# Performance work log

Measured on AMD Instinct MI355X. Metric: run time of the kernel, lower is better.

Reference implementation:

```python
import jax, jax.numpy as jnp
import numpy as np

T = 100.0  # temperature, from init_kwargs
B = 4096
D = 128
NUM_CLASSES = 10


def setup_inputs() -> dict:
    key = jax.random.key(0)
    kx, ky = jax.random.split(key)
    x = jax.random.normal(kx, (B, D), dtype=jnp.float32)
    y = jax.random.randint(ky, (B,), 0, NUM_CLASSES, dtype=jnp.int64)
    return {"x": x, "y": y}


def reference(x, y):
    # Pairwise squared Euclidean distances: dist[i,j] = ||x_i - x_j||^2
    sq = jnp.sum(x * x, axis=1)                      # [b]
    dist = sq[:, None] + sq[None, :] - 2.0 * (x @ x.T)  # [b, b]
    dist = jnp.maximum(dist, 0.0)                    # clamp fp error; diag -> 0

    e = jnp.exp(-dist / T)                           # [b, b]; e[i,i] = 1

    b = x.shape[0]
    same = (y[:, None] == y[None, :])                # same-label mask
    not_self = ~jnp.eye(b, dtype=bool)

    # numerator: sum over j != i with y[j] == y[i]
    num = jnp.sum(jnp.where(same & not_self, e, 0.0), axis=1)  # [b]
    # denominator: sum over ALL j, including j == i (exp(0) = 1), as in the
    # original loop where the denominator accumulates unconditionally
    den = jnp.sum(e, axis=1)                         # [b]

    return jnp.mean(-jnp.log(num / den))
```

## Files before the change

### kernel.cpp

```cpp
#include <hip/hip_runtime.h>
#include <hip/hip_bf16.h>

#define NB 4096

typedef short v8s __attribute__((ext_vector_type(8)));
typedef float v4f __attribute__((ext_vector_type(4)));


__global__ __launch_bounds__(256) void prep_kernel(const float* __restrict__ x,
        float* __restrict__ sq, unsigned short* __restrict__ xb,
        float* __restrict__ out) {
    int tid = threadIdx.x;
    int row = blockIdx.x * 8 + (tid >> 5);
    int lane = tid & 31;
    const float4* xg = (const float4*)x;
    float4 v = xg[row * 32 + lane];
    __hip_bfloat16 h0 = __float2bfloat16(v.x), h1 = __float2bfloat16(v.y);
    __hip_bfloat16 h2 = __float2bfloat16(v.z), h3 = __float2bfloat16(v.w);
    ushort4 u4;
    u4.x = *(unsigned short*)&h0; u4.y = *(unsigned short*)&h1;
    u4.z = *(unsigned short*)&h2; u4.w = *(unsigned short*)&h3;
    ((ushort4*)xb)[row * 32 + lane] = u4;
    float f0 = __bfloat162float(h0), f1 = __bfloat162float(h1);
    float f2 = __bfloat162float(h2), f3 = __bfloat162float(h3);
    float s = f0 * f0 + f1 * f1 + f2 * f2 + f3 * f3;
    #pragma unroll
    for (int off = 16; off > 0; off >>= 1) s += __shfl_down(s, off);
    if (lane == 0) sq[row] = s;
    if (blockIdx.x == 0 && tid == 0) out[0] = 0.f;
}

__global__ __launch_bounds__(512, 4) void snn_mfma(const unsigned short* __restrict__ xb,
        const int* __restrict__ y, const float* __restrict__ sqg,
        float2* __restrict__ part) {
    __shared__ __align__(16) unsigned short At[128 * 136];
    __shared__ __align__(16) unsigned short Bt[128 * 136];
    __shared__ float2 red[2][128];
    __shared__ float sqi[128], sqj[128];
    __shared__ int yi[128], yj[128];

    const int tid = threadIdx.x;
    const int w    = tid >> 6;
    const int lane = tid & 63;
    const int wm = w >> 1;
    const int wn = w & 1;
    const int lr = lane & 15;
    const int q  = lane >> 4;
    const int i0 = blockIdx.x * 128;
    const int j0 = blockIdx.y * 128;

    const v8s* xg = (const v8s*)xb;
    #pragma unroll
    for (int it = 0; it < 4; ++it) {
        int c = it * 512 + tid;
        int row = c >> 4, cc = c & 15;
        *(v8s*)&At[row * 136 + cc * 8] = xg[(i0 + row) * 16 + cc];
        *(v8s*)&Bt[row * 136 + cc * 8] = xg[(j0 + row) * 16 + cc];
    }
    if (tid < 128)      { sqi[tid] = sqg[i0 + tid];       yi[tid] = y[i0 + tid]; }
    else if (tid < 256) { sqj[tid - 128] = sqg[j0 + tid - 128];
                          yj[tid - 128] = y[j0 + tid - 128]; }
    __syncthreads();

    v4f acc[2][4];
    #pragma unroll
    for (int mt = 0; mt < 2; ++mt)
        #pragma unroll
        for (int nt = 0; nt < 4; ++nt)
            #pragma unroll
            for (int r = 0; r < 4; ++r) acc[mt][nt][r] = 0.f;

    #pragma unroll
    for (int kk = 0; kk < 4; ++kk) {
        v8s af[2], bf[4];
        #pragma unroll
        for (int mt = 0; mt < 2; ++mt)
            af[mt] = *(const v8s*)&At[(wm * 32 + mt * 16 + lr) * 136 + kk * 32 + q * 8];
        #pragma unroll
        for (int nt = 0; nt < 4; ++nt)
            bf[nt] = *(const v8s*)&Bt[(wn * 64 + nt * 16 + lr) * 136 + kk * 32 + q * 8];
        #pragma unroll
        for (int mt = 0; mt < 2; ++mt)
            #pragma unroll
            for (int nt = 0; nt < 4; ++nt)
                acc[mt][nt] = __builtin_amdgcn_mfma_f32_16x16x32_bf16(
                    af[mt], bf[nt], acc[mt][nt], 0, 0, 0);
    }

    const float c1 = 0.014426950408889634f;
    const float c2 = 0.028853900817778936f;
    float bj[4]; int yj_r[4], jg[4];
    #pragma unroll
    for (int nt = 0; nt < 4; ++nt) {
        int jc = wn * 64 + nt * 16 + lr;
        bj[nt] = -c1 * sqj[jc]; yj_r[nt] = yj[jc]; jg[nt] = j0 + jc;
    }
    #pragma unroll
    for (int mt = 0; mt < 2; ++mt) {
        #pragma unroll
        for (int r = 0; r < 4; ++r) {
            int rloc = wm * 32 + mt * 16 + q * 4 + r;
            float bi = -c1 * sqi[rloc];
            int yir = yi[rloc], ig = i0 + rloc;
            float n = 0.f, d = 0.f;
            #pragma unroll
            for (int nt = 0; nt < 4; ++nt) {
                float arg = fminf(0.f, fmaf(acc[mt][nt][r], c2, bi + bj[nt]));
                float e = __builtin_amdgcn_exp2f(arg);
                d += e;
                bool ok = (yir == yj_r[nt]) && (ig != jg[nt]);
                n += ok ? e : 0.f;
            }
            n += __shfl_xor(n, 1); d += __shfl_xor(d, 1);
            n += __shfl_xor(n, 2); d += __shfl_xor(d, 2);
            n += __shfl_xor(n, 4); d += __shfl_xor(d, 4);
            n += __shfl_xor(n, 8); d += __shfl_xor(d, 8);
            if (lr == 0) red[wn][rloc] = make_float2(n, d);
        }
    }
    __syncthreads();

    if (tid < 128) {
        float2 a = red[0][tid], b = red[1][tid];
        part[(i0 + tid) * 32 + blockIdx.y] = make_float2(a.x + b.x, a.y + b.y);
    }
}

__global__ __launch_bounds__(256) void snn_final(const float2* __restrict__ part,
        float* __restrict__ out) {
    __shared__ float wsum[4];
    int row = blockIdx.x * 256 + threadIdx.x;
    const float4* p = (const float4*)&part[row * 32];
    float n = 0.f, d = 0.f;
    #pragma unroll
    for (int c = 0; c < 16; ++c) {
        float4 v = p[c];
        n += v.x + v.z; d += v.y + v.w;
    }
    float l = __logf(d) - __logf(n);
    #pragma unroll
    for (int off = 32; off > 0; off >>= 1) l += __shfl_down(l, off);
    int wid = threadIdx.x >> 6;
    if ((threadIdx.x & 63) == 0) wsum[wid] = l;
    __syncthreads();
    if (threadIdx.x == 0) {
        float s = wsum[0] + wsum[1] + wsum[2] + wsum[3];
        atomicAdd(out, s * (1.0f / NB));
    }
}

extern "C" void kernel_launch(void* const* d_in, const int* in_sizes, int n_in,
                              void* d_out, int out_size, void* d_ws, size_t ws_size,
                              hipStream_t stream) {
    const float* x = (const float*)d_in[0];
    const int*   y = (const int*)d_in[1];
    float* out = (float*)d_out;
    float2* part = (float2*)d_ws;
    float* sq = (float*)((char*)d_ws + (1 << 20));
    unsigned short* xb = (unsigned short*)((char*)d_ws + (1 << 20) + (16 << 10));

    prep_kernel<<<NB / 8, 256, 0, stream>>>(x, sq, xb, out);
    dim3 grid(NB / 128, NB / 128);
    snn_mfma<<<grid, 512, 0, stream>>>(xb, y, sq, part);
    snn_final<<<NB / 256, 256, 0, stream>>>(part, out);
}
```

Before: 76.17 us.

## Use direct-to-LDS loads, XOR-swizzled layout, and two j-tiles per block

Xb is now stored with an XOR swizzle on 16-byte chunks, so the LDS tiles need no padding and avoid bank conflicts. Tiles are loaded with global_load_lds DMA instead of going through registers. Each 256-thread block computes a 128x256 strip by reusing the A tile across two B tiles, with a 64x64 register tile per wave. This halves the grid and the partial-sum traffic in exchange for more accumulator registers and serialized B reloads between the two subtiles.

```diff
diff --git a/kernel.cpp b/kernel.cpp
--- a/kernel.cpp
+++ b/kernel.cpp
@@ -6,6 +6,12 @@
 typedef short v8s __attribute__((ext_vector_type(8)));
 typedef float v4f __attribute__((ext_vector_type(4)));
 
+
+__device__ __forceinline__ void dma16(const unsigned short* g, unsigned short* l) {
+    __builtin_amdgcn_global_load_lds(
+        (const __attribute__((address_space(1))) unsigned int*)g,
+        (__attribute__((address_space(3))) unsigned int*)l, 16, 0, 0);
+}
 
 __global__ __launch_bounds__(256) void prep_kernel(const float* __restrict__ x,
         float* __restrict__ sq, unsigned short* __restrict__ xb,
@@ -20,7 +26,9 @@
     ushort4 u4;
     u4.x = *(unsigned short*)&h0; u4.y = *(unsigned short*)&h1;
     u4.z = *(unsigned short*)&h2; u4.w = *(unsigned short*)&h3;
-    ((ushort4*)xb)[row * 32 + lane] = u4;
+    int c = lane >> 1, half = lane & 1;
+    int p = c ^ (row & 15);
+    *(ushort4*)&xb[(size_t)row * 128 + p * 8 + half * 4] = u4;
     float f0 = __bfloat162float(h0), f1 = __bfloat162float(h1);
     float f2 = __bfloat162float(h2), f3 = __bfloat162float(h3);
     float s = f0 * f0 + f1 * f1 + f2 * f2 + f3 * f3;
@@ -30,99 +38,130 @@
     if (blockIdx.x == 0 && tid == 0) out[0] = 0.f;
 }
 
-__global__ __launch_bounds__(512, 4) void snn_mfma(const unsigned short* __restrict__ xb,
+__global__ __launch_bounds__(256) void snn_mfma(const unsigned short* __restrict__ xb,
         const int* __restrict__ y, const float* __restrict__ sqg,
         float2* __restrict__ part) {
-    __shared__ __align__(16) unsigned short At[128 * 136];
-    __shared__ __align__(16) unsigned short Bt[128 * 136];
+    __shared__ __align__(16) unsigned short At[128 * 128];
+    __shared__ __align__(16) unsigned short Bt[128 * 128];
     __shared__ float2 red[2][128];
     __shared__ float sqi[128], sqj[128];
     __shared__ int yi[128], yj[128];
 
     const int tid = threadIdx.x;
-    const int w    = tid >> 6;
-    const int lane = tid & 63;
-    const int wm = w >> 1;
-    const int wn = w & 1;
-    const int lr = lane & 15;
-    const int q  = lane >> 4;
+    const int w = tid >> 6, lane = tid & 63;
+    const int wm = w >> 1, wn = w & 1;
+    const int lr = lane & 15, q = lane >> 4;
     const int i0 = blockIdx.x * 128;
-    const int j0 = blockIdx.y * 128;
-
-    const v8s* xg = (const v8s*)xb;
-    #pragma unroll
-    for (int it = 0; it < 4; ++it) {
-        int c = it * 512 + tid;
-        int row = c >> 4, cc = c & 15;
-        *(v8s*)&At[row * 136 + cc * 8] = xg[(i0 + row) * 16 + cc];
-        *(v8s*)&Bt[row * 136 + cc * 8] = xg[(j0 + row) * 16 + cc];
-    }
-    if (tid < 128)      { sqi[tid] = sqg[i0 + tid];       yi[tid] = y[i0 + tid]; }
-    else if (tid < 256) { sqj[tid - 128] = sqg[j0 + tid - 128];
-                          yj[tid - 128] = y[j0 + tid - 128]; }
+    const int jt0 = blockIdx.y * 2;
+
+    #pragma unroll
+    for (int r = 0; r < 8; ++r) {
+        int row = w * 32 + r * 4;
+        dma16(xb + (size_t)(i0 + row) * 128 + lane * 8, &At[row * 128]);
+        dma16(xb + (size_t)(jt0 * 128 + row) * 128 + lane * 8, &Bt[row * 128]);
+    }
+    if (tid < 128) { sqi[tid] = sqg[i0 + tid]; yi[tid] = y[i0 + tid]; }
+    else { int c = tid - 128; sqj[c] = sqg[jt0 * 128 + c]; yj[c] = y[jt0 * 128 + c]; }
     __syncthreads();
-
-    v4f acc[2][4];
-    #pragma unroll
-    for (int mt = 0; mt < 2; ++mt)
-        #pragma unroll
-        for (int nt = 0; nt < 4; ++nt)
-            #pragma unroll
-            for (int r = 0; r < 4; ++r) acc[mt][nt][r] = 0.f;
-
-    #pragma unroll
-    for (int kk = 0; kk < 4; ++kk) {
-        v8s af[2], bf[4];
-        #pragma unroll
-        for (int mt = 0; mt < 2; ++mt)
-            af[mt] = *(const v8s*)&At[(wm * 32 + mt * 16 + lr) * 136 + kk * 32 + q * 8];
-        #pragma unroll
-        for (int nt = 0; nt < 4; ++nt)
-            bf[nt] = *(const v8s*)&Bt[(wn * 64 + nt * 16 + lr) * 136 + kk * 32 + q * 8];
-        #pragma unroll
-        for (int mt = 0; mt < 2; ++mt)
-            #pragma unroll
-            for (int nt = 0; nt < 4; ++nt)
-                acc[mt][nt] = __builtin_amdgcn_mfma_f32_16x16x32_bf16(
-                    af[mt], bf[nt], acc[mt][nt], 0, 0, 0);
-    }
 
     const float c1 = 0.014426950408889634f;
     const float c2 = 0.028853900817778936f;
-    float bj[4]; int yj_r[4], jg[4];
-    #pragma unroll
-    for (int nt = 0; nt < 4; ++nt) {
-        int jc = wn * 64 + nt * 16 + lr;
-        bj[nt] = -c1 * sqj[jc]; yj_r[nt] = yj[jc]; jg[nt] = j0 + jc;
-    }
-    #pragma unroll
-    for (int mt = 0; mt < 2; ++mt) {
-        #pragma unroll
-        for (int r = 0; r < 4; ++r) {
-            int rloc = wm * 32 + mt * 16 + q * 4 + r;
-            float bi = -c1 * sqi[rloc];
-            int yir = yi[rloc], ig = i0 + rloc;
-            float n = 0.f, d = 0.f;
+    float nsum[4][4], dsum[4][4];
+    #pragma unroll
+    for (int mt = 0; mt < 4; ++mt)
+        #pragma unroll
+        for (int r = 0; r < 4; ++r) { nsum[mt][r] = 0.f; dsum[mt][r] = 0.f; }
+
+    #pragma unroll
+    for (int jt = 0; jt < 2; ++jt) {
+        v4f acc[4][4];
+        #pragma unroll
+        for (int mt = 0; mt < 4; ++mt)
+            #pragma unroll
+            for (int nt = 0; nt < 4; ++nt)
+                #pragma unroll
+                for (int r = 0; r < 4; ++r) acc[mt][nt][r] = 0.f;
+
+        #pragma unroll
+        for (int kk = 0; kk < 4; ++kk) {
+            v8s af[4], bf[4];
+            #pragma unroll
+            for (int mt = 0; mt < 4; ++mt) {
+                int row = wm * 64 + mt * 16 + lr;
+                af[mt] = *(const v8s*)&At[row * 128 + (((kk * 4 + q) ^ lr) * 8)];
+            }
             #pragma unroll
             for (int nt = 0; nt < 4; ++nt) {
-                float arg = fminf(0.f, fmaf(acc[mt][nt][r], c2, bi + bj[nt]));
-                float e = __builtin_amdgcn_exp2f(arg);
-                d += e;
-                bool ok = (yir == yj_r[nt]) && (ig != jg[nt]);
-                n += ok ? e : 0.f;
-            }
-            n += __shfl_xor(n, 1); d += __shfl_xor(d, 1);
-            n += __shfl_xor(n, 2); d += __shfl_xor(d, 2);
-            n += __shfl_xor(n, 4); d += __shfl_xor(d, 4);
-            n += __shfl_xor(n, 8); d += __shfl_xor(d, 8);
-            if (lr == 0) red[wn][rloc] = make_float2(n, d);
-        }
-    }
+                int row = wn * 64 + nt * 16 + lr;
+                bf[nt] = *(const v8s*)&Bt[row * 128 + (((kk * 4 + q) ^ lr) * 8)];
+            }
+            #pragma unroll
+            for (int mt = 0; mt < 4; ++mt)
+                #pragma unroll
+                for (int nt = 0; nt < 4; ++nt)
+                    acc[mt][nt] = __builtin_amdgcn_mfma_f32_16x16x32_bf16(
+                        af[mt], bf[nt], acc[mt][nt], 0, 0, 0);
+        }
+
+        int jbase = (jt0 + jt) * 128;
+        float bj[4]; int yj_r[4], jcol[4];
+        #pragma unroll
+        for (int nt = 0; nt < 4; ++nt) {
+            int jc = wn * 64 + nt * 16 + lr;
+            bj[nt] = -c1 * sqj[jc]; yj_r[nt] = yj[jc]; jcol[nt] = jbase + jc;
+        }
+        #pragma unroll
+        for (int mt = 0; mt < 4; ++mt) {
+            #pragma unroll
+            for (int r = 0; r < 4; ++r) {
+                int rloc = wm * 64 + mt * 16 + q * 4 + r;
+                float bi = -c1 * sqi[rloc];
+                int yir = yi[rloc], ig = i0 + rloc;
+                float n = 0.f, d = 0.f;
+                #pragma unroll
+                for (int nt = 0; nt < 4; ++nt) {
+                    float arg = fminf(0.f, fmaf(acc[mt][nt][r], c2, bi + bj[nt]));
+                    float e = __builtin_amdgcn_exp2f(arg);
+                    d += e;
+                    bool ok = (yir == yj_r[nt]) && (ig != jcol[nt]);
+                    n += ok ? e : 0.f;
+                }
+                n += __shfl_xor(n, 1); d += __shfl_xor(d, 1);
+                n += __shfl_xor(n, 2); d += __shfl_xor(d, 2);
+                n += __shfl_xor(n, 4); d += __shfl_xor(d, 4);
+                n += __shfl_xor(n, 8); d += __shfl_xor(d, 8);
+                nsum[mt][r] += n; dsum[mt][r] += d;
+            }
+        }
+
+        if (jt == 0) {
+            __syncthreads();
+            #pragma unroll
+            for (int r = 0; r < 8; ++r) {
+                int row = w * 32 + r * 4;
+                dma16(xb + (size_t)((jt0 + 1) * 128 + row) * 128 + lane * 8,
+                      &Bt[row * 128]);
+            }
+            if (tid >= 128) {
+                int c = tid - 128;
+                sqj[c] = sqg[(jt0 + 1) * 128 + c]; yj[c] = y[(jt0 + 1) * 128 + c];
+            }
+            __syncthreads();
+        }
+    }
+
+    #pragma unroll
+    for (int mt = 0; mt < 4; ++mt)
+        #pragma unroll
+        for (int r = 0; r < 4; ++r)
+            if (lr == 0)
+                red[wn][wm * 64 + mt * 16 + q * 4 + r] =
+                    make_float2(nsum[mt][r], dsum[mt][r]);
     __syncthreads();
 
     if (tid < 128) {
         float2 a = red[0][tid], b = red[1][tid];
-        part[(i0 + tid) * 32 + blockIdx.y] = make_float2(a.x + b.x, a.y + b.y);
+        part[(size_t)(i0 + tid) * 16 + blockIdx.y] = make_float2(a.x + b.x, a.y + b.y);
     }
 }
 
@@ -130,10 +169,10 @@
         float* __restrict__ out) {
     __shared__ float wsum[4];
     int row = blockIdx.x * 256 + threadIdx.x;
-    const float4* p = (const float4*)&part[row * 32];
+    const float4* p = (const float4*)&part[(size_t)row * 16];
     float n = 0.f, d = 0.f;
     #pragma unroll
-    for (int c = 0; c < 16; ++c) {
+    for (int c = 0; c < 8; ++c) {
         float4 v = p[c];
         n += v.x + v.z; d += v.y + v.w;
     }
@@ -156,11 +195,11 @@
     const int*   y = (const int*)d_in[1];
     float* out = (float*)d_out;
     float2* part = (float2*)d_ws;
-    float* sq = (float*)((char*)d_ws + (1 << 20));
-    unsigned short* xb = (unsigned short*)((char*)d_ws + (1 << 20) + (16 << 10));
+    float* sq = (float*)((char*)d_ws + (512 << 10));
+    unsigned short* xb = (unsigned short*)((char*)d_ws + (512 << 10) + (16 << 10));
 
     prep_kernel<<<NB / 8, 256, 0, stream>>>(x, sq, xb, out);
-    dim3 grid(NB / 128, NB / 128);
-    snn_mfma<<<grid, 512, 0, stream>>>(xb, y, sq, part);
+    dim3 grid(NB / 128, NB / 256);
+    snn_mfma<<<grid, 256, 0, stream>>>(xb, y, sq, part);
     snn_final<<<NB / 256, 256, 0, stream>>>(part, out);
 }
```

Result: no change. 77.60 us (+1.9%).
